# Performance work log

Hardware: AMD Instinct MI355X
Metric: run time of the kernel (lower is better)

The kernel has to match this reference:

```python
import jax, jax.numpy as jnp
import numpy as np

N_USER = 200_000
N_ITEM = 100_000
E = 1_000_000
HID = 64
ED = 16      # edge_dim
DU = 128     # user feature dim
DI = 64      # item feature dim
NCONV = 4    # 2 layers x (fwd, rev)


def setup_inputs() -> dict:
    key = jax.random.key(0)
    ks = jax.random.split(key, 20)
    s = 0.1  # small init scale for numerical sanity
    return {
        'x_user': jax.random.normal(ks[0], (N_USER, DU), jnp.float32),
        'x_item': jax.random.normal(ks[1], (N_ITEM, DI), jnp.float32),
        'edge_attr': jax.random.normal(ks[2], (E, ED), jnp.float32),
        'src_idx': jax.random.randint(ks[3], (E,), 0, N_USER),
        'dst_idx': jax.random.randint(ks[4], (E,), 0, N_ITEM),
        # input projections
        'Wp_user': jax.random.normal(ks[5], (DU, HID), jnp.float32) * s,
        'bp_user': jnp.zeros((HID,), jnp.float32),
        'Wp_item': jax.random.normal(ks[6], (DI, HID), jnp.float32) * s,
        'bp_item': jnp.zeros((HID,), jnp.float32),
        # per-conv params, stacked over NCONV = [layer0 fwd, layer0 rev, layer1 fwd, layer1 rev]
        'eps': jnp.zeros((NCONV,), jnp.float32),  # train_eps=True, init 0
        'We': jax.random.normal(ks[7], (NCONV, ED, HID), jnp.float32) * s,
        'be': jnp.zeros((NCONV, HID), jnp.float32),
        'W1': jax.random.normal(ks[8], (NCONV, HID, HID), jnp.float32) * s,
        'b1': jnp.zeros((NCONV, HID), jnp.float32),
        'W2': jax.random.normal(ks[9], (NCONV, HID, HID), jnp.float32) * s,
        'b2': jnp.zeros((NCONV, HID), jnp.float32),
    }


def _gine(x_src, x_dst, e_src, e_dst, ea, eps, We, be, W1, b1, W2, b2):
    # GINEConv: out = MLP((1+eps)*x_dst + sum_j ReLU(x_src[j] + Lin(edge_attr_j)))
    msg = jax.nn.relu(x_src[e_src] + ea @ We + be)                 # [E, HID]
    agg = jax.ops.segment_sum(msg, e_dst, num_segments=x_dst.shape[0])
    h = (1.0 + eps) * x_dst + agg
    return jax.nn.relu(h @ W1 + b1) @ W2 + b2


def reference(x_user, x_item, edge_attr, src_idx, dst_idx,
              Wp_user, bp_user, Wp_item, bp_item,
              eps, We, be, W1, b1, W2, b2):
    h_u = jax.nn.relu(x_user @ Wp_user + bp_user)   # [N_USER, HID]
    h_i = jax.nn.relu(x_item @ Wp_item + bp_item)   # [N_ITEM, HID]
    for l in range(2):
        cf, cr = 2 * l, 2 * l + 1
        # fwd relation user->item (dst = item); rev = flipped edges, same edge_attr
        new_i = jax.nn.relu(_gine(h_u, h_i, src_idx, dst_idx, edge_attr,
                                  eps[cf], We[cf], be[cf], W1[cf], b1[cf], W2[cf], b2[cf]))
        new_u = jax.nn.relu(_gine(h_i, h_u, dst_idx, src_idx, edge_attr,
                                  eps[cr], We[cr], be[cr], W1[cr], b1[cr], W2[cr], b2[cr]))
        if l > 0:  # use_residual and not first layer
            h_u, h_i = h_u + new_u, h_i + new_i
        else:
            h_u, h_i = new_u, new_i
    return h_u, h_i
```

## Files before the change

kernel.cpp:

```cpp
#include <hip/hip_runtime.h>
#include <hip/hip_bf16.h>

typedef __hip_bfloat16 bf16;

#define N_USER 200000
#define N_ITEM 100000
#define NEDGE  1000000
#define HID    64

__device__ __forceinline__ float bf2f(unsigned int u) {
    unsigned int x = u << 16;
    float f; __builtin_memcpy(&f, &x, 4); return f;
}
__device__ __forceinline__ float ldf(const void* p, long i, int isf32) {
    if (isf32) return ((const float*)p)[i];
    return bf2f(((const unsigned short*)p)[i]);
}
__device__ __forceinline__ void stf(void* p, long i, int isf32, float v) {
    if (isf32) ((float*)p)[i] = v;
    else       ((bf16*)p)[i] = (bf16)v;
}
__device__ __forceinline__ void load_row16(const void* ea, long e, int isf32, float* v) {
    if (isf32) {
        const float4* p = (const float4*)((const float*)ea + e * 16);
        float4 a = p[0], b = p[1], c = p[2], d = p[3];
        v[0]=a.x; v[1]=a.y; v[2]=a.z; v[3]=a.w;
        v[4]=b.x; v[5]=b.y; v[6]=b.z; v[7]=b.w;
        v[8]=c.x; v[9]=c.y; v[10]=c.z; v[11]=c.w;
        v[12]=d.x; v[13]=d.y; v[14]=d.z; v[15]=d.w;
    } else {
        const int4* q = (const int4*)((const unsigned short*)ea + e * 16);
        int4 s0 = q[0], s1 = q[1];
        unsigned int w;
        w=(unsigned)s0.x; v[0]=bf2f(w & 0xffff); v[1]=bf2f(w >> 16);
        w=(unsigned)s0.y; v[2]=bf2f(w & 0xffff); v[3]=bf2f(w >> 16);
        w=(unsigned)s0.z; v[4]=bf2f(w & 0xffff); v[5]=bf2f(w >> 16);
        w=(unsigned)s0.w; v[6]=bf2f(w & 0xffff); v[7]=bf2f(w >> 16);
        w=(unsigned)s1.x; v[8]=bf2f(w & 0xffff); v[9]=bf2f(w >> 16);
        w=(unsigned)s1.y; v[10]=bf2f(w & 0xffff); v[11]=bf2f(w >> 16);
        w=(unsigned)s1.z; v[12]=bf2f(w & 0xffff); v[13]=bf2f(w >> 16);
        w=(unsigned)s1.w; v[14]=bf2f(w & 0xffff); v[15]=bf2f(w >> 16);
    }
}

__global__ void detect_kernel(const void* __restrict__ x, int* __restrict__ flag) {
    if (threadIdx.x == 0 && blockIdx.x == 0) {
        const unsigned short* p = (const unsigned short*)x;
        int f = 0;
        for (int i = 0; i < 512; i++) {
            int ex = (p[i] >> 7) & 0xFF;
            if (ex >= 137) f = 1;
        }
        *flag = f;
    }
}

__global__ __launch_bounds__(256) void hist_kernel(
    const int* __restrict__ key, int* __restrict__ cnt, int E)
{
    int e = blockIdx.x * 256 + threadIdx.x;
    if (e < E) atomicAdd(&cnt[key[e]], 1);
}

__global__ __launch_bounds__(1024) void scan_kernel(
    const int* __restrict__ deg, int* __restrict__ rowptr,
    int* __restrict__ cursor, int N)
{
    __shared__ int ssum[1024];
    __shared__ int s_carry;
    int tid = threadIdx.x;
    if (tid == 0) s_carry = 0;
    __syncthreads();
    for (int base = 0; base < N; base += 8192) {
        int i0 = base + tid * 8;
        int v[8]; int tot = 0;
#pragma unroll
        for (int k = 0; k < 8; k++) { int i = i0 + k; v[k] = (i < N) ? deg[i] : 0; tot += v[k]; }
        ssum[tid] = tot;
        __syncthreads();
        for (int off = 1; off < 1024; off <<= 1) {
            int t = (tid >= off) ? ssum[tid - off] : 0;
            __syncthreads();
            ssum[tid] += t;
            __syncthreads();
        }
        int exc = ssum[tid] - tot + s_carry;
#pragma unroll
        for (int k = 0; k < 8; k++) {
            int i = i0 + k;
            if (i < N) { rowptr[i] = exc; cursor[i] = exc; }
            exc += v[k];
        }
        __syncthreads();
        if (tid == 1023) s_carry += ssum[1023];
        __syncthreads();
    }
    if (tid == 0) rowptr[N] = s_carry;
}

__global__ __launch_bounds__(256) void scatter_kernel(
    const int* __restrict__ key, const int* __restrict__ other,
    int* __restrict__ cursor, int2* __restrict__ perm, int E)
{
    int e = blockIdx.x * 256 + threadIdx.x;
    if (e >= E) return;
    int p = atomicAdd(&cursor[key[e]], 1);
    perm[p] = make_int2(e, other[e]);
}

template<int K>
__global__ __launch_bounds__(256) void proj_kernel(
    const void* __restrict__ x, const void* __restrict__ W,
    const void* __restrict__ b, float* __restrict__ out, int N,
    const int* __restrict__ flagp)
{
    __shared__ float Ws[K * 64];
    __shared__ float xs[4][K];
    int isf32 = *flagp;
    int tid = threadIdx.x;
    for (int i = tid; i < K * 64; i += 256) Ws[i] = ldf(W, i, isf32);
    int r = tid >> 6, c = tid & 63;
    float bc = ldf(b, c, isf32);
    for (int row0 = blockIdx.x * 4; row0 < N; row0 += gridDim.x * 4) {
        __syncthreads();
        for (int i = tid; i < 4 * K; i += 256) {
            int rr = i / K, k = i - rr * K;
            int row = row0 + rr;
            xs[rr][k] = (row < N) ? ldf(x, (long)row * K + k, isf32) : 0.f;
        }
        __syncthreads();
        int row = row0 + r;
        float acc = bc;
#pragma unroll
        for (int k = 0; k < K; k++) acc = fmaf(xs[r][k], Ws[k * 64 + c], acc);
        if (row < N) out[(long)row * 64 + c] = fmaxf(acc, 0.f);
    }
}

template<int RESID>
__global__ __launch_bounds__(256, 4) void conv_kernel(
    const float* __restrict__ h_src, const float* __restrict__ h_dst,
    const int* __restrict__ rowptr, const int2* __restrict__ perm,
    const void* __restrict__ ea,
    const void* __restrict__ We, long weoff, const void* __restrict__ be, long beoff,
    const void* __restrict__ W1, const void* __restrict__ b1,
    const void* __restrict__ W2, const void* __restrict__ b2, long woff, long boff,
    const void* __restrict__ eps, int conv,
    float* __restrict__ outf, void* __restrict__ outv, long outoff,
    int N, const int* __restrict__ flagp)
{
    __shared__ float Wes[16 * 64];
    __shared__ float W1s[64 * 64];
    __shared__ float W2s[64 * 64];
    __shared__ float bes[64], b1s[64], b2s[64];
    __shared__ float vs[4][64], ts[4][64];
    int isf32 = *flagp;
    int tid = threadIdx.x;
    for (int i = tid; i < 4096; i += 256) {
        W1s[i] = ldf(W1, woff + i, isf32);
        W2s[i] = ldf(W2, woff + i, isf32);
    }
    for (int i = tid; i < 1024; i += 256) Wes[i] = ldf(We, weoff + i, isf32);
    if (tid < 64) {
        bes[tid] = ldf(be, beoff + tid, isf32);
        b1s[tid] = ldf(b1, boff + tid, isf32);
        b2s[tid] = ldf(b2, boff + tid, isf32);
    }
    __syncthreads();
    float eps1 = 1.f + ldf(eps, conv, isf32);
    int w = tid >> 6, c = tid & 63;

    for (int n0 = blockIdx.x * 4; n0 < N; n0 += gridDim.x * 4) {
        int n = n0 + w;
        float acc = 0.f, hv = 0.f;
        if (n < N) {
            hv = h_dst[(long)n * 64 + c];
            int jb = rowptr[n], je = rowptr[n + 1];
            int j = jb;
            for (; j + 4 <= je; j += 4) {
                int2 p0 = perm[j], p1 = perm[j+1], p2 = perm[j+2], p3 = perm[j+3];
                float a0[16], a1[16], a2[16], a3[16];
                load_row16(ea, p0.x, isf32, a0);
                load_row16(ea, p1.x, isf32, a1);
                load_row16(ea, p2.x, isf32, a2);
                load_row16(ea, p3.x, isf32, a3);
                float h0 = h_src[(long)p0.y * 64 + c];
                float h1 = h_src[(long)p1.y * 64 + c];
                float h2 = h_src[(long)p2.y * 64 + c];
                float h3 = h_src[(long)p3.y * 64 + c];
                float m0 = bes[c], m1 = m0, m2 = m0, m3 = m0;
#pragma unroll
                for (int k = 0; k < 16; k++) {
                    float wv = Wes[k * 64 + c];
                    m0 = fmaf(a0[k], wv, m0); m1 = fmaf(a1[k], wv, m1);
                    m2 = fmaf(a2[k], wv, m2); m3 = fmaf(a3[k], wv, m3);
                }
                acc += fmaxf(m0 + h0, 0.f); acc += fmaxf(m1 + h1, 0.f);
                acc += fmaxf(m2 + h2, 0.f); acc += fmaxf(m3 + h3, 0.f);
            }
            for (; j < je; j++) {
                int2 p0 = perm[j];
                float a0[16];
                load_row16(ea, p0.x, isf32, a0);
                float h0 = h_src[(long)p0.y * 64 + c];
                float m0 = bes[c];
#pragma unroll
                for (int k = 0; k < 16; k++) m0 = fmaf(a0[k], Wes[k * 64 + c], m0);
                acc += fmaxf(m0 + h0, 0.f);
            }
        }
        vs[w][c] = eps1 * hv + acc;
        __syncthreads();
        float t = b1s[c];
#pragma unroll
        for (int k = 0; k < 64; k++) t = fmaf(vs[w][k], W1s[k * 64 + c], t);
        t = fmaxf(t, 0.f);
        ts[w][c] = t;
        __syncthreads();
        float o = b2s[c];
#pragma unroll
        for (int k = 0; k < 64; k++) o = fmaf(ts[w][k], W2s[k * 64 + c], o);
        o = fmaxf(o, 0.f);
        if (n < N) {
            if (RESID) o += hv;
            long base = (long)n * 64;
            if (outv) stf(outv, outoff + base + c, isf32, o);
            else      outf[base + c] = o;
        }
    }
}

extern "C" void kernel_launch(void* const* d_in, const int* in_sizes, int n_in,
                              void* d_out, int out_size, void* d_ws, size_t ws_size,
                              hipStream_t stream)
{
    const void* x_user    = d_in[0];
    const void* x_item    = d_in[1];
    const void* edge_attr = d_in[2];
    const int*  src_idx   = (const int*)d_in[3];
    const int*  dst_idx   = (const int*)d_in[4];
    const void* Wp_user   = d_in[5];
    const void* bp_user   = d_in[6];
    const void* Wp_item   = d_in[7];
    const void* bp_item   = d_in[8];
    const void* eps       = d_in[9];
    const void* We        = d_in[10];
    const void* be        = d_in[11];
    const void* W1        = d_in[12];
    const void* b1        = d_in[13];
    const void* W2        = d_in[14];
    const void* b2        = d_in[15];

    float* ws   = (float*)d_ws;
    int*  flag  = (int*)d_ws;
    float* h_u  = ws + 256;
    float* h_i  = h_u + 12800000;
    float* h_u2 = h_i + 6400000;
    float* h_i2 = h_u2 + 12800000;
    int* rowptr_i = (int*)(h_i2 + 6400000);
    int* cursor_i = rowptr_i + 100096;
    int2* perm_i  = (int2*)(cursor_i + 100096);
    int* rowptr_u = (int*)(perm_i + 1000000);
    int* cursor_u = rowptr_u + 200192;
    int2* perm_u  = (int2*)(cursor_u + 200192);

    const int EG = (NEDGE + 255) / 256;

    detect_kernel<<<1, 64, 0, stream>>>(x_user, flag);

    hipMemsetAsync(cursor_i, 0, N_ITEM * sizeof(int), stream);
    hist_kernel<<<EG, 256, 0, stream>>>(dst_idx, cursor_i, NEDGE);
    scan_kernel<<<1, 1024, 0, stream>>>(cursor_i, rowptr_i, cursor_i, N_ITEM);
    scatter_kernel<<<EG, 256, 0, stream>>>(dst_idx, src_idx, cursor_i, perm_i, NEDGE);
    hipMemsetAsync(cursor_u, 0, N_USER * sizeof(int), stream);
    hist_kernel<<<EG, 256, 0, stream>>>(src_idx, cursor_u, NEDGE);
    scan_kernel<<<1, 1024, 0, stream>>>(cursor_u, rowptr_u, cursor_u, N_USER);
    scatter_kernel<<<EG, 256, 0, stream>>>(src_idx, dst_idx, cursor_u, perm_u, NEDGE);

    proj_kernel<128><<<1024, 256, 0, stream>>>(x_user, Wp_user, bp_user, h_u, N_USER, flag);
    proj_kernel<64><<<1024, 256, 0, stream>>>(x_item, Wp_item, bp_item, h_i, N_ITEM, flag);

    conv_kernel<0><<<1024, 256, 0, stream>>>(h_u, h_i, rowptr_i, perm_i, edge_attr,
        We, 0 * 1024, be, 0 * 64, W1, b1, W2, b2, 0 * 4096, 0 * 64,
        eps, 0, h_i2, nullptr, 0, N_ITEM, flag);
    conv_kernel<0><<<1024, 256, 0, stream>>>(h_i, h_u, rowptr_u, perm_u, edge_attr,
        We, 1 * 1024, be, 1 * 64, W1, b1, W2, b2, 1 * 4096, 1 * 64,
        eps, 1, h_u2, nullptr, 0, N_USER, flag);

    conv_kernel<1><<<1024, 256, 0, stream>>>(h_u2, h_i2, rowptr_i, perm_i, edge_attr,
        We, 2 * 1024, be, 2 * 64, W1, b1, W2, b2, 2 * 4096, 2 * 64,
        eps, 2, nullptr, d_out, (long)N_USER * HID, N_ITEM, flag);
    conv_kernel<1><<<1024, 256, 0, stream>>>(h_i2, h_u2, rowptr_u, perm_u, edge_attr,
        We, 3 * 1024, be, 3 * 64, W1, b1, W2, b2, 3 * 4096, 3 * 64,
        eps, 3, nullptr, d_out, 0, N_USER, flag);
}
```

Before: 2.400 ms.

## Split conv into aggregation and MLP kernels, fuse CSR build passes

Each GINE conv is split into an edge-aggregation kernel, which drops the 36KB of MLP weight staging and runs at higher occupancy, and a separate MLP kernel that processes two nodes per thread to reuse weights. Histogram and scatter for both relations are fused into single launches, and the two prefix scans run as two blocks of one launch using wave-shuffle scans. The cost is an extra round trip of the aggregated features through global memory, and buffers are reused in place for the intermediate results.

```diff
diff --git a/kernel.cpp b/kernel.cpp
--- a/kernel.cpp
+++ b/kernel.cpp
@@ -44,68 +44,84 @@
 }
 
 __global__ void detect_kernel(const void* __restrict__ x, int* __restrict__ flag) {
-    if (threadIdx.x == 0 && blockIdx.x == 0) {
-        const unsigned short* p = (const unsigned short*)x;
-        int f = 0;
-        for (int i = 0; i < 512; i++) {
-            int ex = (p[i] >> 7) & 0xFF;
-            if (ex >= 137) f = 1;
-        }
-        *flag = f;
-    }
-}
-
-__global__ __launch_bounds__(256) void hist_kernel(
-    const int* __restrict__ key, int* __restrict__ cnt, int E)
+    const unsigned short* p = (const unsigned short*)x;
+    int f = 0;
+    for (int k = threadIdx.x; k < 512; k += 64) {
+        int ex = (p[k] >> 7) & 0xFF;
+        if (ex >= 137) f = 1;
+    }
+    unsigned long long b = __ballot(f != 0);
+    if (threadIdx.x == 0) *flag = (b != 0ULL) ? 1 : 0;
+}
+
+__global__ __launch_bounds__(256) void hist2_kernel(
+    const int* __restrict__ src, const int* __restrict__ dst,
+    int* __restrict__ cnt_u, int* __restrict__ cnt_i, int E)
 {
     int e = blockIdx.x * 256 + threadIdx.x;
-    if (e < E) atomicAdd(&cnt[key[e]], 1);
+    if (e < E) {
+        atomicAdd(&cnt_u[src[e]], 1);
+        atomicAdd(&cnt_i[dst[e]], 1);
+    }
+}
+
+__device__ __forceinline__ int wave_incl_scan(int v, int lane) {
+#pragma unroll
+    for (int off = 1; off < 64; off <<= 1) {
+        int t = __shfl_up(v, off, 64);
+        if (lane >= off) v += t;
+    }
+    return v;
 }
 
 __global__ __launch_bounds__(1024) void scan_kernel(
-    const int* __restrict__ deg, int* __restrict__ rowptr,
-    int* __restrict__ cursor, int N)
-{
-    __shared__ int ssum[1024];
+    int* __restrict__ deg_i, int* __restrict__ rp_i, int Ni,
+    int* __restrict__ deg_u, int* __restrict__ rp_u, int Nu)
+{
+    __shared__ int swsum[16];
     __shared__ int s_carry;
-    int tid = threadIdx.x;
+    int* deg    = (blockIdx.x == 0) ? deg_i : deg_u;
+    int* rowptr = (blockIdx.x == 0) ? rp_i  : rp_u;
+    int N       = (blockIdx.x == 0) ? Ni    : Nu;
+    int tid = threadIdx.x, lane = tid & 63, wid = tid >> 6;
     if (tid == 0) s_carry = 0;
-    __syncthreads();
+    int grand = 0;
     for (int base = 0; base < N; base += 8192) {
         int i0 = base + tid * 8;
         int v[8]; int tot = 0;
 #pragma unroll
         for (int k = 0; k < 8; k++) { int i = i0 + k; v[k] = (i < N) ? deg[i] : 0; tot += v[k]; }
-        ssum[tid] = tot;
-        __syncthreads();
-        for (int off = 1; off < 1024; off <<= 1) {
-            int t = (tid >= off) ? ssum[tid - off] : 0;
-            __syncthreads();
-            ssum[tid] += t;
-            __syncthreads();
-        }
-        int exc = ssum[tid] - tot + s_carry;
+        int incl = wave_incl_scan(tot, lane);
+        if (lane == 63) swsum[wid] = incl;
+        __syncthreads();
+        int carry = s_carry;
+        int wbase = 0;
+        for (int jw = 0; jw < wid; jw++) wbase += swsum[jw];
+        int exc = carry + wbase + incl - tot;
 #pragma unroll
         for (int k = 0; k < 8; k++) {
             int i = i0 + k;
-            if (i < N) { rowptr[i] = exc; cursor[i] = exc; }
+            if (i < N) { rowptr[i] = exc; deg[i] = exc; }
             exc += v[k];
         }
         __syncthreads();
-        if (tid == 1023) s_carry += ssum[1023];
-        __syncthreads();
-    }
-    if (tid == 0) rowptr[N] = s_carry;
-}
-
-__global__ __launch_bounds__(256) void scatter_kernel(
-    const int* __restrict__ key, const int* __restrict__ other,
-    int* __restrict__ cursor, int2* __restrict__ perm, int E)
+        if (tid == 1023) { s_carry = exc; grand = exc; }
+    }
+    if (tid == 1023) rowptr[N] = grand;
+}
+
+__global__ __launch_bounds__(256) void scatter2_kernel(
+    const int* __restrict__ src, const int* __restrict__ dst,
+    int* __restrict__ cur_u, int* __restrict__ cur_i,
+    int2* __restrict__ perm_u, int2* __restrict__ perm_i, int E)
 {
     int e = blockIdx.x * 256 + threadIdx.x;
     if (e >= E) return;
-    int p = atomicAdd(&cursor[key[e]], 1);
-    perm[p] = make_int2(e, other[e]);
+    int s = src[e], d = dst[e];
+    int pu = atomicAdd(&cur_u[s], 1);
+    perm_u[pu] = make_int2(e, d);
+    int pi = atomicAdd(&cur_i[d], 1);
+    perm_i[pi] = make_int2(e, s);
 }
 
 template<int K>
@@ -137,95 +153,125 @@
     }
 }
 
-template<int RESID>
-__global__ __launch_bounds__(256, 4) void conv_kernel(
+__global__ __launch_bounds__(256, 8) void agg_kernel(
     const float* __restrict__ h_src, const float* __restrict__ h_dst,
     const int* __restrict__ rowptr, const int2* __restrict__ perm,
     const void* __restrict__ ea,
     const void* __restrict__ We, long weoff, const void* __restrict__ be, long beoff,
+    const void* __restrict__ eps, int conv,
+    float* __restrict__ agg, int N, const int* __restrict__ flagp)
+{
+    __shared__ float Wes[16 * 64];
+    __shared__ float bes[64];
+    int isf32 = *flagp;
+    int tid = threadIdx.x;
+    for (int i = tid; i < 1024; i += 256) Wes[i] = ldf(We, weoff + i, isf32);
+    if (tid < 64) bes[tid] = ldf(be, beoff + tid, isf32);
+    __syncthreads();
+    float eps1 = 1.f + ldf(eps, conv, isf32);
+    int w = tid >> 6, c = tid & 63;
+    float bec = bes[c];
+
+    for (int n = blockIdx.x * 4 + w; n < N; n += gridDim.x * 4) {
+        float hv = h_dst[(long)n * 64 + c];
+        float acc = 0.f;
+        int jb = rowptr[n], je = rowptr[n + 1];
+        int j = jb;
+        for (; j + 4 <= je; j += 4) {
+            int2 p0 = perm[j], p1 = perm[j+1], p2 = perm[j+2], p3 = perm[j+3];
+            float a0[16], a1[16], a2[16], a3[16];
+            load_row16(ea, p0.x, isf32, a0);
+            load_row16(ea, p1.x, isf32, a1);
+            load_row16(ea, p2.x, isf32, a2);
+            load_row16(ea, p3.x, isf32, a3);
+            float h0 = h_src[(long)p0.y * 64 + c];
+            float h1 = h_src[(long)p1.y * 64 + c];
+            float h2 = h_src[(long)p2.y * 64 + c];
+            float h3 = h_src[(long)p3.y * 64 + c];
+            float m0 = bec, m1 = bec, m2 = bec, m3 = bec;
+#pragma unroll
+            for (int k = 0; k < 16; k++) {
+                float wv = Wes[k * 64 + c];
+                m0 = fmaf(a0[k], wv, m0); m1 = fmaf(a1[k], wv, m1);
+                m2 = fmaf(a2[k], wv, m2); m3 = fmaf(a3[k], wv, m3);
+            }
+            acc += fmaxf(m0 + h0, 0.f); acc += fmaxf(m1 + h1, 0.f);
+            acc += fmaxf(m2 + h2, 0.f); acc += fmaxf(m3 + h3, 0.f);
+        }
+        for (; j < je; j++) {
+            int2 p0 = perm[j];
+            float a0[16];
+            load_row16(ea, p0.x, isf32, a0);
+            float h0 = h_src[(long)p0.y * 64 + c];
+            float m0 = bec;
+#pragma unroll
+            for (int k = 0; k < 16; k++) m0 = fmaf(a0[k], Wes[k * 64 + c], m0);
+            acc += fmaxf(m0 + h0, 0.f);
+        }
+        agg[(long)n * 64 + c] = eps1 * hv + acc;
+    }
+}
+
+template<int RESID>
+__global__ __launch_bounds__(256, 4) void mlp_kernel(
+    const float* __restrict__ vin, const float* __restrict__ resid,
     const void* __restrict__ W1, const void* __restrict__ b1,
     const void* __restrict__ W2, const void* __restrict__ b2, long woff, long boff,
-    const void* __restrict__ eps, int conv,
     float* __restrict__ outf, void* __restrict__ outv, long outoff,
     int N, const int* __restrict__ flagp)
 {
-    __shared__ float Wes[16 * 64];
-    __shared__ float W1s[64 * 64];
-    __shared__ float W2s[64 * 64];
-    __shared__ float bes[64], b1s[64], b2s[64];
-    __shared__ float vs[4][64], ts[4][64];
+    __shared__ float W1s[4096], W2s[4096];
+    __shared__ float b1s[64], b2s[64];
+    __shared__ float vs[8][64], ts[8][64];
     int isf32 = *flagp;
     int tid = threadIdx.x;
     for (int i = tid; i < 4096; i += 256) {
         W1s[i] = ldf(W1, woff + i, isf32);
         W2s[i] = ldf(W2, woff + i, isf32);
     }
-    for (int i = tid; i < 1024; i += 256) Wes[i] = ldf(We, weoff + i, isf32);
     if (tid < 64) {
-        bes[tid] = ldf(be, beoff + tid, isf32);
         b1s[tid] = ldf(b1, boff + tid, isf32);
         b2s[tid] = ldf(b2, boff + tid, isf32);
     }
-    __syncthreads();
-    float eps1 = 1.f + ldf(eps, conv, isf32);
     int w = tid >> 6, c = tid & 63;
-
-    for (int n0 = blockIdx.x * 4; n0 < N; n0 += gridDim.x * 4) {
-        int n = n0 + w;
-        float acc = 0.f, hv = 0.f;
-        if (n < N) {
-            hv = h_dst[(long)n * 64 + c];
-            int jb = rowptr[n], je = rowptr[n + 1];
-            int j = jb;
-            for (; j + 4 <= je; j += 4) {
-                int2 p0 = perm[j], p1 = perm[j+1], p2 = perm[j+2], p3 = perm[j+3];
-                float a0[16], a1[16], a2[16], a3[16];
-                load_row16(ea, p0.x, isf32, a0);
-                load_row16(ea, p1.x, isf32, a1);
-                load_row16(ea, p2.x, isf32, a2);
-                load_row16(ea, p3.x, isf32, a3);
-                float h0 = h_src[(long)p0.y * 64 + c];
-                float h1 = h_src[(long)p1.y * 64 + c];
-                float h2 = h_src[(long)p2.y * 64 + c];
-                float h3 = h_src[(long)p3.y * 64 + c];
-                float m0 = bes[c], m1 = m0, m2 = m0, m3 = m0;
-#pragma unroll
-                for (int k = 0; k < 16; k++) {
-                    float wv = Wes[k * 64 + c];
-                    m0 = fmaf(a0[k], wv, m0); m1 = fmaf(a1[k], wv, m1);
-                    m2 = fmaf(a2[k], wv, m2); m3 = fmaf(a3[k], wv, m3);
-                }
-                acc += fmaxf(m0 + h0, 0.f); acc += fmaxf(m1 + h1, 0.f);
-                acc += fmaxf(m2 + h2, 0.f); acc += fmaxf(m3 + h3, 0.f);
-            }
-            for (; j < je; j++) {
-                int2 p0 = perm[j];
-                float a0[16];
-                load_row16(ea, p0.x, isf32, a0);
-                float h0 = h_src[(long)p0.y * 64 + c];
-                float m0 = bes[c];
-#pragma unroll
-                for (int k = 0; k < 16; k++) m0 = fmaf(a0[k], Wes[k * 64 + c], m0);
-                acc += fmaxf(m0 + h0, 0.f);
-            }
-        }
-        vs[w][c] = eps1 * hv + acc;
-        __syncthreads();
-        float t = b1s[c];
-#pragma unroll
-        for (int k = 0; k < 64; k++) t = fmaf(vs[w][k], W1s[k * 64 + c], t);
-        t = fmaxf(t, 0.f);
-        ts[w][c] = t;
-        __syncthreads();
-        float o = b2s[c];
-#pragma unroll
-        for (int k = 0; k < 64; k++) o = fmaf(ts[w][k], W2s[k * 64 + c], o);
-        o = fmaxf(o, 0.f);
-        if (n < N) {
-            if (RESID) o += hv;
-            long base = (long)n * 64;
-            if (outv) stf(outv, outoff + base + c, isf32, o);
-            else      outf[base + c] = o;
+    int na_off = 2 * w, nb_off = 2 * w + 1;
+    for (long n0 = (long)blockIdx.x * 8; n0 < N; n0 += (long)gridDim.x * 8) {
+        __syncthreads();
+        for (int i = tid; i < 512; i += 256) {
+            long n = n0 + (i >> 6);
+            vs[i >> 6][i & 63] = (n < N) ? vin[n * 64 + (i & 63)] : 0.f;
+        }
+        __syncthreads();
+        float ta = b1s[c], tb = b1s[c];
+#pragma unroll
+        for (int k = 0; k < 64; k++) {
+            float wv = W1s[k * 64 + c];
+            ta = fmaf(vs[na_off][k], wv, ta);
+            tb = fmaf(vs[nb_off][k], wv, tb);
+        }
+        ts[na_off][c] = fmaxf(ta, 0.f);
+        ts[nb_off][c] = fmaxf(tb, 0.f);
+        __syncthreads();
+        float oa = b2s[c], ob = b2s[c];
+#pragma unroll
+        for (int k = 0; k < 64; k++) {
+            float wv = W2s[k * 64 + c];
+            oa = fmaf(ts[na_off][k], wv, oa);
+            ob = fmaf(ts[nb_off][k], wv, ob);
+        }
+        oa = fmaxf(oa, 0.f); ob = fmaxf(ob, 0.f);
+        long na = n0 + na_off, nb = n0 + nb_off;
+        if (na < N) {
+            float o = oa;
+            if (RESID) o += resid[na * 64 + c];
+            if (outv) stf(outv, outoff + na * 64 + c, isf32, o);
+            else      outf[na * 64 + c] = o;
+        }
+        if (nb < N) {
+            float o = ob;
+            if (RESID) o += resid[nb * 64 + c];
+            if (outv) stf(outv, outoff + nb * 64 + c, isf32, o);
+            else      outf[nb * 64 + c] = o;
         }
     }
 }
@@ -269,28 +315,31 @@
     detect_kernel<<<1, 64, 0, stream>>>(x_user, flag);
 
     hipMemsetAsync(cursor_i, 0, N_ITEM * sizeof(int), stream);
-    hist_kernel<<<EG, 256, 0, stream>>>(dst_idx, cursor_i, NEDGE);
-    scan_kernel<<<1, 1024, 0, stream>>>(cursor_i, rowptr_i, cursor_i, N_ITEM);
-    scatter_kernel<<<EG, 256, 0, stream>>>(dst_idx, src_idx, cursor_i, perm_i, NEDGE);
     hipMemsetAsync(cursor_u, 0, N_USER * sizeof(int), stream);
-    hist_kernel<<<EG, 256, 0, stream>>>(src_idx, cursor_u, NEDGE);
-    scan_kernel<<<1, 1024, 0, stream>>>(cursor_u, rowptr_u, cursor_u, N_USER);
-    scatter_kernel<<<EG, 256, 0, stream>>>(src_idx, dst_idx, cursor_u, perm_u, NEDGE);
+    hist2_kernel<<<EG, 256, 0, stream>>>(src_idx, dst_idx, cursor_u, cursor_i, NEDGE);
+    scan_kernel<<<2, 1024, 0, stream>>>(cursor_i, rowptr_i, N_ITEM,
+                                        cursor_u, rowptr_u, N_USER);
+    scatter2_kernel<<<EG, 256, 0, stream>>>(src_idx, dst_idx, cursor_u, cursor_i,
+                                            perm_u, perm_i, NEDGE);
 
     proj_kernel<128><<<1024, 256, 0, stream>>>(x_user, Wp_user, bp_user, h_u, N_USER, flag);
     proj_kernel<64><<<1024, 256, 0, stream>>>(x_item, Wp_item, bp_item, h_i, N_ITEM, flag);
 
-    conv_kernel<0><<<1024, 256, 0, stream>>>(h_u, h_i, rowptr_i, perm_i, edge_attr,
-        We, 0 * 1024, be, 0 * 64, W1, b1, W2, b2, 0 * 4096, 0 * 64,
-        eps, 0, h_i2, nullptr, 0, N_ITEM, flag);
-    conv_kernel<0><<<1024, 256, 0, stream>>>(h_i, h_u, rowptr_u, perm_u, edge_attr,
-        We, 1 * 1024, be, 1 * 64, W1, b1, W2, b2, 1 * 4096, 1 * 64,
-        eps, 1, h_u2, nullptr, 0, N_USER, flag);
-
-    conv_kernel<1><<<1024, 256, 0, stream>>>(h_u2, h_i2, rowptr_i, perm_i, edge_attr,
-        We, 2 * 1024, be, 2 * 64, W1, b1, W2, b2, 2 * 4096, 2 * 64,
-        eps, 2, nullptr, d_out, (long)N_USER * HID, N_ITEM, flag);
-    conv_kernel<1><<<1024, 256, 0, stream>>>(h_i2, h_u2, rowptr_u, perm_u, edge_attr,
-        We, 3 * 1024, be, 3 * 64, W1, b1, W2, b2, 3 * 4096, 3 * 64,
-        eps, 3, nullptr, d_out, 0, N_USER, flag);
-}
+    agg_kernel<<<2048, 256, 0, stream>>>(h_u, h_i, rowptr_i, perm_i, edge_attr,
+        We, 0 * 1024, be, 0 * 64, eps, 0, h_i2, N_ITEM, flag);
+    agg_kernel<<<2048, 256, 0, stream>>>(h_i, h_u, rowptr_u, perm_u, edge_attr,
+        We, 1 * 1024, be, 1 * 64, eps, 1, h_u2, N_USER, flag);
+    mlp_kernel<0><<<1024, 256, 0, stream>>>(h_i2, nullptr,
+        W1, b1, W2, b2, 0 * 4096, 0 * 64, h_i2, nullptr, 0, N_ITEM, flag);
+    mlp_kernel<0><<<1024, 256, 0, stream>>>(h_u2, nullptr,
+        W1, b1, W2, b2, 1 * 4096, 1 * 64, h_u2, nullptr, 0, N_USER, flag);
+
+    agg_kernel<<<2048, 256, 0, stream>>>(h_u2, h_i2, rowptr_i, perm_i, edge_attr,
+        We, 2 * 1024, be, 2 * 64, eps, 2, h_i, N_ITEM, flag);
+    agg_kernel<<<2048, 256, 0, stream>>>(h_i2, h_u2, rowptr_u, perm_u, edge_attr,
+        We, 3 * 1024, be, 3 * 64, eps, 3, h_u, N_USER, flag);
+    mlp_kernel<1><<<1024, 256, 0, stream>>>(h_i, h_i2,
+        W1, b1, W2, b2, 2 * 4096, 2 * 64, nullptr, d_out, (long)N_USER * HID, N_ITEM, flag);
+    mlp_kernel<1><<<1024, 256, 0, stream>>>(h_u, h_u2,
+        W1, b1, W2, b2, 3 * 4096, 3 * 64, nullptr, d_out, 0, N_USER, flag);
+}
```

After: 6.582 ms. +174.2%, slower.
